# Kernel tuning notes

Hardware: AMD Instinct MI355X
Metric: run time of the kernel (lower is better)

Reference implementation:

```python
import jax, jax.numpy as jnp
import numpy as np

D, H, E, K, DF = 1024, 16, 8, 2, 4096
HD = D // H


def setup_inputs() -> dict:
    key = jax.random.key(0)
    ks = jax.random.split(key, 16)
    s = 0.02
    return {
        "x": jax.random.normal(ks[0], (8, 1024, D), jnp.float32),
        "ln1_g": jnp.ones((D,), jnp.float32),
        "ln1_b": jnp.zeros((D,), jnp.float32),
        "Wqkv": jax.random.normal(ks[1], (D, 3 * D), jnp.float32) * s,
        "bqkv": jnp.zeros((3 * D,), jnp.float32),
        "Wo": jax.random.normal(ks[2], (D, D), jnp.float32) * s,
        "bo": jnp.zeros((D,), jnp.float32),
        "ln2_g": jnp.ones((D,), jnp.float32),
        "ln2_b": jnp.zeros((D,), jnp.float32),
        "Wr": jax.random.normal(ks[3], (D, E), jnp.float32) * s,
        "W1": jax.random.normal(ks[4], (E, D, DF), jnp.float32) * s,
        "b1": jnp.zeros((E, DF), jnp.float32),
        "W2": jax.random.normal(ks[5], (E, DF, D), jnp.float32) * s,
        "b2": jnp.zeros((E, D), jnp.float32),
    }


def _ln(x, g, b, eps=1e-5):
    mu = jnp.mean(x, axis=-1, keepdims=True)
    var = jnp.var(x, axis=-1, keepdims=True)
    return (x - mu) * jax.lax.rsqrt(var + eps) * g + b


def reference(x, ln1_g, ln1_b, Wqkv, bqkv, Wo, bo, ln2_g, ln2_b, Wr, W1, b1, W2, b2):
    B, S, _ = x.shape
    # ---- pre-norm multi-head attention ----
    n1 = _ln(x, ln1_g, ln1_b)
    qkv = n1 @ Wqkv + bqkv  # [B,S,3D]
    q, k, v = jnp.split(qkv, 3, axis=-1)
    q = q.reshape(B, S, H, HD).transpose(0, 2, 1, 3)
    k = k.reshape(B, S, H, HD).transpose(0, 2, 1, 3)
    v = v.reshape(B, S, H, HD).transpose(0, 2, 1, 3)
    scores = jnp.einsum("bhqd,bhkd->bhqk", q, k) / np.sqrt(HD).astype(np.float32)
    attn = jax.nn.softmax(scores, axis=-1)
    ao = jnp.einsum("bhqk,bhkd->bhqd", attn, v)
    ao = ao.transpose(0, 2, 1, 3).reshape(B, S, D) @ Wo + bo
    x = x + ao  # residual (dropout=0)

    # ---- pre-norm MoE FFN ----
    n2 = _ln(x, ln2_g, ln2_b).reshape(B * S, D)  # [T,D]
    logits = n2 @ Wr  # [T,E]
    probs = jax.nn.softmax(logits, axis=-1)
    topv, topi = jax.lax.top_k(probs, K)  # [T,K]
    topv = topv / jnp.sum(topv, axis=-1, keepdims=True)
    onehot = jax.nn.one_hot(topi, E, dtype=probs.dtype)  # [T,K,E]
    gates = jnp.einsum("tke,tk->te", onehot, topv)  # dense sparse gates [T,E]

    # dense dispatch: each expert's FFN weighted by its gate (zero for unrouted)
    moe = jnp.zeros_like(n2)
    for e in range(E):
        h = jax.nn.gelu(n2 @ W1[e] + b1[e])
        moe = moe + gates[:, e:e + 1] * (h @ W2[e] + b2[e])
    x = x + moe.reshape(B, S, D)

    # load-balancing aux loss: E * sum(frac_routed_e * mean_prob_e)
    frac = jnp.mean(jnp.sum(onehot, axis=1), axis=0) / K  # [E]
    aux = E * jnp.sum(frac * jnp.mean(probs, axis=0))
    return x, aux
```

## Files before the change

### kernel.cpp

```cpp
#include <hip/hip_runtime.h>
#include <cstdint>
#include <cstddef>

using u16 = unsigned short;
using u32 = unsigned int;
typedef __attribute__((ext_vector_type(8))) short bf16x8;
typedef __attribute__((ext_vector_type(4))) float f32x4;

#define T_TOK 8192
#define SEQ   1024
#define NHEAD 16

__device__ __forceinline__ u16 f2b(float f) {
  u32 u = __float_as_uint(f);
  u32 r = (u + 0x7FFFu + ((u >> 16) & 1u)) >> 16;
  return (u16)r;
}
__device__ __forceinline__ float b2f(u16 u) {
  return __uint_as_float(((u32)u) << 16);
}

__global__ __launch_bounds__(256)
void k_cast_transpose(const float* __restrict__ in, u16* __restrict__ out, int R, int C) {
  __shared__ float tile[32][33];
  int bc = blockIdx.x * 32, br = blockIdx.y * 32;
  size_t bofs = (size_t)blockIdx.z * R * C;
  in += bofs; out += bofs;
  int tx = threadIdx.x, ty = threadIdx.y;
  for (int i = 0; i < 32; i += 8)
    tile[ty + i][tx] = in[(size_t)(br + ty + i) * C + bc + tx];
  __syncthreads();
  for (int i = 0; i < 32; i += 8)
    out[(size_t)(bc + ty + i) * R + br + tx] = f2b(tile[tx][ty + i]);
}

__global__ __launch_bounds__(256)
void k_ln(const float* __restrict__ x, const float* __restrict__ g, const float* __restrict__ b,
          u16* __restrict__ out) {
  int row = blockIdx.x, t = threadIdx.x;
  float4 v = ((const float4*)(x + (size_t)row * 1024))[t];
  float s  = v.x + v.y + v.z + v.w;
  float ss = v.x * v.x + v.y * v.y + v.z * v.z + v.w * v.w;
  for (int d = 1; d < 64; d <<= 1) { s += __shfl_xor(s, d); ss += __shfl_xor(ss, d); }
  __shared__ float sm[8];
  int w = t >> 6, lane = t & 63;
  if (lane == 0) { sm[w] = s; sm[4 + w] = ss; }
  __syncthreads();
  s = sm[0] + sm[1] + sm[2] + sm[3];
  ss = sm[4] + sm[5] + sm[6] + sm[7];
  float mu = s * (1.f / 1024.f);
  float var = ss * (1.f / 1024.f) - mu * mu;
  float inv = rsqrtf(var + 1e-5f);
  float4 gv = ((const float4*)g)[t];
  float4 bv = ((const float4*)b)[t];
  u32 lo = (u32)f2b((v.x - mu) * inv * gv.x + bv.x) | ((u32)f2b((v.y - mu) * inv * gv.y + bv.y) << 16);
  u32 hi = (u32)f2b((v.z - mu) * inv * gv.z + bv.z) | ((u32)f2b((v.w - mu) * inv * gv.w + bv.w) << 16);
  u32* dst = (u32*)(out + (size_t)row * 1024 + t * 4);
  dst[0] = lo; dst[1] = hi;
}

template<int MODE, bool EXPERT, bool GATHER>
__global__ __launch_bounds__(256)
void k_gemm(const u16* __restrict__ A, const u16* __restrict__ BT,
            const float* __restrict__ bias, const float* __restrict__ res,
            void* __restrict__ Cout, int M, int N, int Kd, int ldA,
            const int* __restrict__ off, const int* __restrict__ rows) {
  int z = EXPERT ? blockIdx.z : 0;
  int m_base = 0, M_local = M;
  if (EXPERT) { m_base = off[z]; M_local = off[z + 1] - m_base; }
  int by = blockIdx.y, bx = blockIdx.x;
  if (by * 128 >= M_local) return;
  if (EXPERT) { BT += (size_t)z * N * Kd; bias += (size_t)z * N; }

  __shared__ u16 As[128][40];
  __shared__ u16 Bs[128][40];

  int t = threadIdx.x;
  int lane = t & 63, w = t >> 6;
  int wm = w >> 1, wn = w & 1;
  int lr = lane & 15, lk = (lane >> 4) * 8;

  f32x4 acc[4][4] = {};

  int sr = t >> 1;
  int sc = (t & 1) * 16;
  int mr = by * 128 + sr;
  int mclamp = mr < M_local - 1 ? mr : M_local - 1;
  size_t arow = GATHER ? (size_t)rows[m_base + mclamp] : (size_t)(m_base + mclamp);
  const u16* aptr = A + arow * (size_t)ldA + sc;
  const u16* bptr = BT + (size_t)(bx * 128 + sr) * Kd + sc;

  for (int k0 = 0; k0 < Kd; k0 += 32) {
    int4 av0 = *(const int4*)(aptr + k0);
    int4 av1 = *(const int4*)(aptr + k0 + 8);
    int4 bv0 = *(const int4*)(bptr + k0);
    int4 bv1 = *(const int4*)(bptr + k0 + 8);
    __syncthreads();
    *(int4*)&As[sr][sc] = av0; *(int4*)&As[sr][sc + 8] = av1;
    *(int4*)&Bs[sr][sc] = bv0; *(int4*)&Bs[sr][sc + 8] = bv1;
    __syncthreads();
    bf16x8 af[4], bfr[4];
#pragma unroll
    for (int m = 0; m < 4; m++) af[m] = *(const bf16x8*)&As[wm * 64 + m * 16 + lr][lk];
#pragma unroll
    for (int n = 0; n < 4; n++) bfr[n] = *(const bf16x8*)&Bs[wn * 64 + n * 16 + lr][lk];
#pragma unroll
    for (int m = 0; m < 4; m++)
#pragma unroll
      for (int n = 0; n < 4; n++)
        acc[m][n] = __builtin_amdgcn_mfma_f32_16x16x32_bf16(af[m], bfr[n], acc[m][n], 0, 0, 0);
  }

  int cr = (lane >> 4) * 4, cc = lane & 15;
#pragma unroll
  for (int m = 0; m < 4; m++) {
    int rl = by * 128 + wm * 64 + m * 16 + cr;
#pragma unroll
    for (int n = 0; n < 4; n++) {
      int col = bx * 128 + wn * 64 + n * 16 + cc;
      float bia = bias[col];
#pragma unroll
      for (int r = 0; r < 4; r++) {
        int rr = rl + r;
        if (rr >= M_local) continue;
        size_t row = (size_t)(m_base + rr);
        float v = acc[m][n][r] + bia;
        if (MODE == 0) {
          ((u16*)Cout)[row * N + col] = f2b(v);
        } else if (MODE == 1) {
          ((float*)Cout)[row * N + col] = v + res[row * N + col];
        } else if (MODE == 2) {
          float x3 = v * v * v;
          float ge = 0.5f * v * (1.f + tanhf(0.7978845608028654f * (v + 0.044715f * x3)));
          ((u16*)Cout)[row * N + col] = f2b(ge);
        } else {
          ((float*)Cout)[row * N + col] = v;
        }
      }
    }
  }
}

__global__ __launch_bounds__(256)
void k_attn(const u16* __restrict__ qkv, u16* __restrict__ ao) {
  __shared__ u16 Kt[64][72];
  __shared__ u16 Vt[64][72];
  __shared__ u16 Pl[4][16][72];

  int bh = blockIdx.y;
  int b = bh >> 4, h = bh & 15;
  int q0 = blockIdx.x * 64;
  int t = threadIdx.x, lane = t & 63, w = t >> 6;
  int lr = lane & 15, lk = (lane >> 4) * 8;

  int tq = b * SEQ + q0 + w * 16 + lr;
  const u16* qrow = qkv + (size_t)tq * 3072 + h * 64;
  bf16x8 qf[2];
#pragma unroll
  for (int kk = 0; kk < 2; kk++) {
    bf16x8 raw = *(const bf16x8*)(qrow + kk * 32 + lk);
#pragma unroll
    for (int j = 0; j < 8; j++) raw[j] = (short)f2b(b2f((u16)raw[j]) * 0.125f);
    qf[kk] = raw;
  }

  float m[4], l[4];
  f32x4 o[4];
#pragma unroll
  for (int r = 0; r < 4; r++) { m[r] = -1e30f; l[r] = 0.f; }
#pragma unroll
  for (int c = 0; c < 4; c++) o[c] = (f32x4){0.f, 0.f, 0.f, 0.f};

  int key_r = t >> 2;
  int key_c = (t & 3) * 16;

  for (int kv0 = 0; kv0 < SEQ; kv0 += 64) {
    int tk = b * SEQ + kv0 + key_r;
    const u16* krow = qkv + (size_t)tk * 3072 + 1024 + h * 64 + key_c;
    const u16* vrow = qkv + (size_t)tk * 3072 + 2048 + h * 64 + key_c;
    int4 ka = *(const int4*)krow;
    int4 kb = *(const int4*)(krow + 8);
    int4 vv4[2];
    vv4[0] = *(const int4*)vrow;
    vv4[1] = *(const int4*)(vrow + 8);
    const u16* vv = (const u16*)vv4;
    __syncthreads();
    *(int4*)&Kt[key_r][key_c] = ka;
    *(int4*)&Kt[key_r][key_c + 8] = kb;
#pragma unroll
    for (int j = 0; j < 16; j++) Vt[key_c + j][key_r] = vv[j];
    __syncthreads();

    f32x4 s[4];
#pragma unroll
    for (int n = 0; n < 4; n++) {
      s[n] = (f32x4){0.f, 0.f, 0.f, 0.f};
#pragma unroll
      for (int kk = 0; kk < 2; kk++) {
        bf16x8 kf = *(const bf16x8*)&Kt[n * 16 + lr][kk * 32 + lk];
        s[n] = __builtin_amdgcn_mfma_f32_16x16x32_bf16(qf[kk], kf, s[n], 0, 0, 0);
      }
    }
    float alpha[4], rsum[4];
#pragma unroll
    for (int r = 0; r < 4; r++) {
      float mx = fmaxf(fmaxf(s[0][r], s[1][r]), fmaxf(s[2][r], s[3][r]));
#pragma unroll
      for (int d = 1; d < 16; d <<= 1) mx = fmaxf(mx, __shfl_xor(mx, d));
      float mn = fmaxf(m[r], mx);
      alpha[r] = expf(m[r] - mn);
      m[r] = mn;
      rsum[r] = 0.f;
    }
#pragma unroll
    for (int n = 0; n < 4; n++)
#pragma unroll
      for (int r = 0; r < 4; r++) {
        float p = expf(s[n][r] - m[r]);
        rsum[r] += p;
        Pl[w][(lane >> 4) * 4 + r][n * 16 + lr] = f2b(p);
      }
#pragma unroll
    for (int r = 0; r < 4; r++) {
      float rs = rsum[r];
#pragma unroll
      for (int d = 1; d < 16; d <<= 1) rs += __shfl_xor(rs, d);
      l[r] = l[r] * alpha[r] + rs;
#pragma unroll
      for (int c = 0; c < 4; c++) o[c][r] *= alpha[r];
    }
    bf16x8 pa[2];
#pragma unroll
    for (int kk = 0; kk < 2; kk++) pa[kk] = *(const bf16x8*)&Pl[w][lr][kk * 32 + lk];
#pragma unroll
    for (int c = 0; c < 4; c++)
#pragma unroll
      for (int kk = 0; kk < 2; kk++) {
        bf16x8 vf = *(const bf16x8*)&Vt[c * 16 + lr][kk * 32 + lk];
        o[c] = __builtin_amdgcn_mfma_f32_16x16x32_bf16(pa[kk], vf, o[c], 0, 0, 0);
      }
  }

  int cr = (lane >> 4) * 4, cc = lane & 15;
#pragma unroll
  for (int r = 0; r < 4; r++) {
    float invl = 1.f / l[r];
    int trow = b * SEQ + q0 + w * 16 + cr + r;
#pragma unroll
    for (int c = 0; c < 4; c++)
      ao[(size_t)trow * 1024 + h * 64 + c * 16 + cc] = f2b(o[c][r] * invl);
  }
}

__global__ __launch_bounds__(256)
void k_router(const float* __restrict__ x1, const float* __restrict__ g, const float* __restrict__ b,
              const float* __restrict__ Wr, int* __restrict__ topi, float* __restrict__ topv,
              int* __restrict__ cnt_part, float* __restrict__ sp_part) {
  __shared__ int lcnt[8];
  __shared__ float lsp[8];
  int t = threadIdx.x, w = t >> 6, lane = t & 63;
  if (t < 8) { lcnt[t] = 0; lsp[t] = 0.f; }
  __syncthreads();

  float gv[16], bv[16];
#pragma unroll
  for (int i = 0; i < 4; i++) {
    float4 g4 = ((const float4*)g)[lane * 4 + i];
    float4 b4 = ((const float4*)b)[lane * 4 + i];
    gv[i * 4 + 0] = g4.x; gv[i * 4 + 1] = g4.y; gv[i * 4 + 2] = g4.z; gv[i * 4 + 3] = g4.w;
    bv[i * 4 + 0] = b4.x; bv[i * 4 + 1] = b4.y; bv[i * 4 + 2] = b4.z; bv[i * 4 + 3] = b4.w;
  }
  float wr[16][8];
#pragma unroll
  for (int j = 0; j < 16; j++) {
    float4 w0 = ((const float4*)Wr)[(lane * 16 + j) * 2];
    float4 w1 = ((const float4*)Wr)[(lane * 16 + j) * 2 + 1];
    wr[j][0] = w0.x; wr[j][1] = w0.y; wr[j][2] = w0.z; wr[j][3] = w0.w;
    wr[j][4] = w1.x; wr[j][5] = w1.y; wr[j][6] = w1.z; wr[j][7] = w1.w;
  }

  for (int i = 0; i < 8; i++) {
    int row = blockIdx.x * 32 + w * 8 + i;
    const float4* xr = (const float4*)(x1 + (size_t)row * 1024);
    float xv[16];
    float s = 0.f, ss = 0.f;
#pragma unroll
    for (int q = 0; q < 4; q++) {
      float4 v = xr[lane * 4 + q];
      xv[q * 4 + 0] = v.x; xv[q * 4 + 1] = v.y; xv[q * 4 + 2] = v.z; xv[q * 4 + 3] = v.w;
      s += v.x + v.y + v.z + v.w;
      ss += v.x * v.x + v.y * v.y + v.z * v.z + v.w * v.w;
    }
#pragma unroll
    for (int d = 1; d < 64; d <<= 1) { s += __shfl_xor(s, d); ss += __shfl_xor(ss, d); }
    float mu = s * (1.f / 1024.f);
    float var = ss * (1.f / 1024.f) - mu * mu;
    float inv = rsqrtf(var + 1e-5f);
    float p[8] = {};
#pragma unroll
    for (int j = 0; j < 16; j++) {
      float n = (xv[j] - mu) * inv * gv[j] + bv[j];
#pragma unroll
      for (int e = 0; e < 8; e++) p[e] += n * wr[j][e];
    }
#pragma unroll
    for (int e = 0; e < 8; e++)
#pragma unroll
      for (int d = 1; d < 64; d <<= 1) p[e] += __shfl_xor(p[e], d);
    if (lane == 0) {
      float mx = p[0];
#pragma unroll
      for (int e = 1; e < 8; e++) mx = fmaxf(mx, p[e]);
      float ex[8], sum = 0.f;
#pragma unroll
      for (int e = 0; e < 8; e++) { ex[e] = expf(p[e] - mx); sum += ex[e]; }
      float pr[8];
#pragma unroll
      for (int e = 0; e < 8; e++) pr[e] = ex[e] / sum;
      int i0 = 0; float b0 = pr[0];
      for (int e = 1; e < 8; e++) if (pr[e] > b0) { b0 = pr[e]; i0 = e; }
      int i1 = -1; float b1 = -1.f;
      for (int e = 0; e < 8; e++) if (e != i0 && pr[e] > b1) { b1 = pr[e]; i1 = e; }
      float inv2 = 1.f / (b0 + b1);
      topi[row * 2] = i0; topi[row * 2 + 1] = i1;
      topv[row * 2] = b0 * inv2; topv[row * 2 + 1] = b1 * inv2;
      atomicAdd(&lcnt[i0], 1); atomicAdd(&lcnt[i1], 1);
#pragma unroll
      for (int e = 0; e < 8; e++) atomicAdd(&lsp[e], pr[e]);
    }
  }
  __syncthreads();
  if (t < 8) {
    cnt_part[blockIdx.x * 8 + t] = lcnt[t];
    sp_part[blockIdx.x * 8 + t] = lsp[t];
  }
}

__global__ void k_scan_aux(const int* __restrict__ cnt_part, const float* __restrict__ sp_part,
                           int* __restrict__ off, int* __restrict__ cursor, float* __restrict__ aux_out) {
  __shared__ int csum[8];
  __shared__ float ssum[8];
  int t = threadIdx.x;
  int e = t & 7, ch = t >> 3;
  int c = 0; float s = 0.f;
  for (int i = ch * 32; i < ch * 32 + 32; i++) { c += cnt_part[i * 8 + e]; s += sp_part[i * 8 + e]; }
#pragma unroll
  for (int d = 8; d < 64; d <<= 1) { c += __shfl_xor(c, d); s += __shfl_xor(s, d); }
  if (t < 8) { csum[t] = c; ssum[t] = s; }
  __syncthreads();
  if (t == 0) {
    int o = 0;
    for (int q = 0; q < 8; q++) { off[q] = o; cursor[q] = o; o += csum[q]; }
    off[8] = o;
    float aux = 0.f;
    for (int q = 0; q < 8; q++)
      aux += ((float)csum[q] / (float)(T_TOK * 2)) * (ssum[q] / (float)T_TOK);
    aux_out[0] = 8.f * aux;
  }
}

__global__ __launch_bounds__(256)
void k_scatter(const int* __restrict__ topi, int* __restrict__ cursor,
               int* __restrict__ rows, int* __restrict__ slot_of) {
  __shared__ int hist[8];
  __shared__ int base[8];
  int t = threadIdx.x;
  if (t < 8) hist[t] = 0;
  __syncthreads();
  int tok = blockIdx.x * 256 + t;
  int e0 = topi[tok * 2], e1 = topi[tok * 2 + 1];
  int r0 = atomicAdd(&hist[e0], 1);
  int r1 = atomicAdd(&hist[e1], 1);
  __syncthreads();
  if (t < 8) base[t] = atomicAdd(&cursor[t], hist[t]);
  __syncthreads();
  int p0 = base[e0] + r0, p1 = base[e1] + r1;
  rows[p0] = tok; rows[p1] = tok;
  slot_of[tok * 2] = p0; slot_of[tok * 2 + 1] = p1;
}

__global__ __launch_bounds__(256)
void k_combine(const float* __restrict__ x1, const float* __restrict__ out2,
               const int* __restrict__ slot_of, const float* __restrict__ topv,
               float* __restrict__ out) {
  int row = blockIdx.x, t = threadIdx.x;
  int s0 = slot_of[row * 2], s1 = slot_of[row * 2 + 1];
  float w0 = topv[row * 2], w1 = topv[row * 2 + 1];
  float4 a  = ((const float4*)(x1 + (size_t)row * 1024))[t];
  float4 e0 = ((const float4*)(out2 + (size_t)s0 * 1024))[t];
  float4 e1 = ((const float4*)(out2 + (size_t)s1 * 1024))[t];
  float4 r;
  r.x = a.x + w0 * e0.x + w1 * e1.x;
  r.y = a.y + w0 * e0.y + w1 * e1.y;
  r.z = a.z + w0 * e0.z + w1 * e1.z;
  r.w = a.w + w0 * e0.w + w1 * e1.w;
  ((float4*)(out + (size_t)row * 1024))[t] = r;
}

extern "C" void kernel_launch(void* const* d_in, const int* in_sizes, int n_in,
                              void* d_out, int out_size, void* d_ws, size_t ws_size,
                              hipStream_t stream) {
  const float* x    = (const float*)d_in[0];
  const float* ln1g = (const float*)d_in[1];
  const float* ln1b = (const float*)d_in[2];
  const float* Wqkv = (const float*)d_in[3];
  const float* bqkv = (const float*)d_in[4];
  const float* Wo   = (const float*)d_in[5];
  const float* bo   = (const float*)d_in[6];
  const float* ln2g = (const float*)d_in[7];
  const float* ln2b = (const float*)d_in[8];
  const float* Wr   = (const float*)d_in[9];
  const float* W1   = (const float*)d_in[10];
  const float* b1   = (const float*)d_in[11];
  const float* W2   = (const float*)d_in[12];
  const float* b2   = (const float*)d_in[13];
  float* out = (float*)d_out;

  char* wp = (char*)d_ws;
  auto alloc = [&](size_t bytes) -> void* {
    void* p = (void*)wp;
    wp += (bytes + 255) & ~(size_t)255;
    return p;
  };
  u16*   WqkvT = (u16*)alloc((size_t)3072 * 1024 * 2);
  u16*   WoT   = (u16*)alloc((size_t)1024 * 1024 * 2);
  u16*   W1T   = (u16*)alloc((size_t)8 * 4096 * 1024 * 2);
  u16*   W2T   = (u16*)alloc((size_t)8 * 1024 * 4096 * 2);
  u16*   n1    = (u16*)alloc((size_t)8192 * 1024 * 2);
  u16*   qkv   = (u16*)alloc((size_t)8192 * 3072 * 2);
  u16*   aob   = (u16*)alloc((size_t)8192 * 1024 * 2);
  float* x1    = (float*)alloc((size_t)8192 * 1024 * 4);
  u16*   n2b   = (u16*)alloc((size_t)8192 * 1024 * 2);
  u16*   hbuf  = (u16*)alloc((size_t)16384 * 4096 * 2);
  float* out2  = (float*)alloc((size_t)16384 * 1024 * 4);
  int*   topi  = (int*)alloc((size_t)8192 * 2 * 4);
  float* topv  = (float*)alloc((size_t)8192 * 2 * 4);
  int*   rowsl = (int*)alloc((size_t)16384 * 4);
  int*   slot  = (int*)alloc((size_t)16384 * 4);
  int*   cntp  = (int*)alloc((size_t)256 * 8 * 4);
  float* spp   = (float*)alloc((size_t)256 * 8 * 4);
  int*   offs  = (int*)alloc(256);
  int*   curs  = (int*)alloc(256);

  k_cast_transpose<<<dim3(96, 32, 1), dim3(32, 8), 0, stream>>>(Wqkv, WqkvT, 1024, 3072);
  k_cast_transpose<<<dim3(32, 32, 1), dim3(32, 8), 0, stream>>>(Wo, WoT, 1024, 1024);
  k_cast_transpose<<<dim3(128, 32, 8), dim3(32, 8), 0, stream>>>(W1, W1T, 1024, 4096);
  k_cast_transpose<<<dim3(32, 128, 8), dim3(32, 8), 0, stream>>>(W2, W2T, 4096, 1024);

  k_ln<<<8192, 256, 0, stream>>>(x, ln1g, ln1b, n1);
  k_gemm<0, false, false><<<dim3(24, 64, 1), 256, 0, stream>>>(
      n1, WqkvT, bqkv, nullptr, qkv, 8192, 3072, 1024, 1024, nullptr, nullptr);
  k_attn<<<dim3(16, 128), 256, 0, stream>>>(qkv, aob);
  k_gemm<1, false, false><<<dim3(8, 64, 1), 256, 0, stream>>>(
      aob, WoT, bo, x, x1, 8192, 1024, 1024, 1024, nullptr, nullptr);

  k_ln<<<8192, 256, 0, stream>>>(x1, ln2g, ln2b, n2b);
  k_router<<<256, 256, 0, stream>>>(x1, ln2g, ln2b, Wr, topi, topv, cntp, spp);
  k_scan_aux<<<1, 64, 0, stream>>>(cntp, spp, offs, curs, out + 8388608);
  k_scatter<<<32, 256, 0, stream>>>(topi, curs, rowsl, slot);

  k_gemm<2, true, true><<<dim3(32, 64, 8), 256, 0, stream>>>(
      n2b, W1T, b1, nullptr, hbuf, 0, 4096, 1024, 1024, offs, rowsl);
  k_gemm<3, true, false><<<dim3(8, 64, 8), 256, 0, stream>>>(
      hbuf, W2T, b2, nullptr, out2, 0, 1024, 4096, 4096, offs, nullptr);
  k_combine<<<8192, 256, 0, stream>>>(x1, out2, slot, topv, out);
}
```

Measured before the change: 1.024 ms.

## Double-buffer GEMM tiles via direct global-to-LDS loads with XOR swizzle

Replaces the register-staged global-to-shared copy in the shared GEMM kernel with `global_load_lds` direct loads into a double-buffered LDS tile. The next K-slice is prefetched while MFMAs run on the current one, and one barrier per iteration replaces two. It uses an XOR swizzle in place of row padding to avoid LDS bank conflicts. It also rewrites the tanh-based GELU as the equivalent sigmoid form using `__expf`, which is cheaper but slightly less exact.

```diff
diff --git a/kernel.cpp b/kernel.cpp
--- a/kernel.cpp
+++ b/kernel.cpp
@@ -72,43 +72,65 @@
   if (by * 128 >= M_local) return;
   if (EXPERT) { BT += (size_t)z * N * Kd; bias += (size_t)z * N; }
 
-  __shared__ u16 As[128][40];
-  __shared__ u16 Bs[128][40];
+  __shared__ alignas(1024) u16 As[2][4096];
+  __shared__ alignas(1024) u16 Bs[2][4096];
 
   int t = threadIdx.x;
   int lane = t & 63, w = t >> 6;
   int wm = w >> 1, wn = w & 1;
-  int lr = lane & 15, lk = (lane >> 4) * 8;
+  int lr = lane & 15;
+  int slot = lane >> 4;
+  int sx = (slot ^ ((lr >> 1) & 3)) << 3;
+
+  int ssrc = (lane & 3) ^ ((lane >> 3) & 3);
+  const u16* aG[2]; const u16* bG[2];
+  u16* aL[2]; u16* bL[2];
+#pragma unroll
+  for (int c = 0; c < 2; c++) {
+    int chunk = 2 * w + c;
+    int rl = chunk * 16 + (lane >> 2);
+    int mr = by * 128 + rl;
+    int mc = mr < M_local - 1 ? mr : M_local - 1;
+    size_t arow = GATHER ? (size_t)rows[m_base + mc] : (size_t)(m_base + mc);
+    aG[c] = A + arow * (size_t)ldA + ssrc * 8;
+    bG[c] = BT + (size_t)(bx * 128 + rl) * Kd + ssrc * 8;
+    aL[c] = &As[0][chunk * 512];
+    bL[c] = &Bs[0][chunk * 512];
+  }
+
+  auto stage = [&](int k0, int buf) {
+#pragma unroll
+    for (int c = 0; c < 2; c++) {
+      __builtin_amdgcn_global_load_lds(
+          (const __attribute__((address_space(1))) void*)(aG[c] + k0),
+          (__attribute__((address_space(3))) void*)(aL[c] + buf * 4096), 16, 0, 0);
+      __builtin_amdgcn_global_load_lds(
+          (const __attribute__((address_space(1))) void*)(bG[c] + k0),
+          (__attribute__((address_space(3))) void*)(bL[c] + buf * 4096), 16, 0, 0);
+    }
+  };
 
   f32x4 acc[4][4] = {};
 
-  int sr = t >> 1;
-  int sc = (t & 1) * 16;
-  int mr = by * 128 + sr;
-  int mclamp = mr < M_local - 1 ? mr : M_local - 1;
-  size_t arow = GATHER ? (size_t)rows[m_base + mclamp] : (size_t)(m_base + mclamp);
-  const u16* aptr = A + arow * (size_t)ldA + sc;
-  const u16* bptr = BT + (size_t)(bx * 128 + sr) * Kd + sc;
-
+  stage(0, 0);
+  __syncthreads();
+  int cur = 0;
   for (int k0 = 0; k0 < Kd; k0 += 32) {
-    int4 av0 = *(const int4*)(aptr + k0);
-    int4 av1 = *(const int4*)(aptr + k0 + 8);
-    int4 bv0 = *(const int4*)(bptr + k0);
-    int4 bv1 = *(const int4*)(bptr + k0 + 8);
-    __syncthreads();
-    *(int4*)&As[sr][sc] = av0; *(int4*)&As[sr][sc + 8] = av1;
-    *(int4*)&Bs[sr][sc] = bv0; *(int4*)&Bs[sr][sc + 8] = bv1;
-    __syncthreads();
+    if (k0 + 32 < Kd) stage(k0 + 32, cur ^ 1);
     bf16x8 af[4], bfr[4];
 #pragma unroll
-    for (int m = 0; m < 4; m++) af[m] = *(const bf16x8*)&As[wm * 64 + m * 16 + lr][lk];
-#pragma unroll
-    for (int n = 0; n < 4; n++) bfr[n] = *(const bf16x8*)&Bs[wn * 64 + n * 16 + lr][lk];
+    for (int m = 0; m < 4; m++)
+      af[m] = *(const bf16x8*)&As[cur][(wm * 64 + m * 16 + lr) * 32 + sx];
+#pragma unroll
+    for (int n = 0; n < 4; n++)
+      bfr[n] = *(const bf16x8*)&Bs[cur][(wn * 64 + n * 16 + lr) * 32 + sx];
 #pragma unroll
     for (int m = 0; m < 4; m++)
 #pragma unroll
       for (int n = 0; n < 4; n++)
         acc[m][n] = __builtin_amdgcn_mfma_f32_16x16x32_bf16(af[m], bfr[n], acc[m][n], 0, 0, 0);
+    __syncthreads();
+    cur ^= 1;
   }
 
   int cr = (lane >> 4) * 4, cc = lane & 15;
@@ -130,8 +152,8 @@
         } else if (MODE == 1) {
           ((float*)Cout)[row * N + col] = v + res[row * N + col];
         } else if (MODE == 2) {
-          float x3 = v * v * v;
-          float ge = 0.5f * v * (1.f + tanhf(0.7978845608028654f * (v + 0.044715f * x3)));
+          float u = v + 0.044715f * v * v * v;
+          float ge = v / (1.f + __expf(-1.5957691216057308f * u));
           ((u16*)Cout)[row * N + col] = f2b(ge);
         } else {
           ((float*)Cout)[row * N + col] = v;
```

After: 935.9 us. -8.6%, faster.
